# Performance work log

Hardware: AMD Instinct MI355X
Metric: run time of the kernel (lower is better)

The kernel has to match this reference:

```python
import jax, jax.numpy as jnp
import numpy as np

N_NODES = 100000
N_EDGES = 3200000
D_IN = 256
D_HID = 256
D_OUT = 64


def setup_inputs() -> dict:
    key = jax.random.key(0)
    k1, k2, k3, k4 = jax.random.split(key, 4)
    x = jax.random.normal(k1, (N_NODES, D_IN), dtype=jnp.float32)
    edge_index = jax.random.randint(k2, (2, N_EDGES), 0, N_NODES, dtype=jnp.int32)
    W1 = jax.random.normal(k3, (D_IN, D_HID), dtype=jnp.float32) / np.sqrt(D_IN)
    b1 = jnp.zeros((D_HID,), dtype=jnp.float32)
    W2 = jax.random.normal(k4, (D_HID, D_OUT), dtype=jnp.float32) / np.sqrt(D_HID)
    b2 = jnp.zeros((D_OUT,), dtype=jnp.float32)
    return {"x": x, "edge_index": edge_index, "W1": W1, "b1": b1, "W2": W2, "b2": b2}


def _gcn_conv(x, src, dst, norm, W, b, n_nodes):
    # dense linear transform, then normalized scatter-add aggregation
    h = x @ W  # [N, out]
    msg = norm[:, None] * h[src]  # gather + scale, [E+N, out]
    out = jax.ops.segment_sum(msg, dst, num_segments=n_nodes)
    return out + b


def reference(x, edge_index, W1, b1, W2, b2):
    n = x.shape[0]
    # add self-loops (PyG GCNConv default)
    loops = jnp.arange(n, dtype=edge_index.dtype)
    src = jnp.concatenate([edge_index[0], loops])
    dst = jnp.concatenate([edge_index[1], loops])
    # symmetric normalization deg^{-1/2}[src] * deg^{-1/2}[dst]
    deg = jax.ops.segment_sum(jnp.ones_like(src, dtype=x.dtype), dst, num_segments=n)
    dinv = jnp.where(deg > 0, jax.lax.rsqrt(jnp.maximum(deg, 1.0)), 0.0)
    norm = dinv[src] * dinv[dst]

    h = _gcn_conv(x, src, dst, norm, W1, b1, n)
    h = jax.nn.relu(h)
    # dropout is identity at inference
    h = _gcn_conv(h, src, dst, norm, W2, b2, n)
    return jax.nn.log_softmax(h, axis=1)
```

## Files before the change

kernel.cpp:

```cpp
#include <hip/hip_runtime.h>
#include <hip/hip_bf16.h>


typedef __bf16 bf16;
typedef bf16 bf16x4 __attribute__((ext_vector_type(4)));
typedef bf16 bf16x8 __attribute__((ext_vector_type(8)));
typedef float f32x4 __attribute__((ext_vector_type(4)));
typedef signed char s8;
typedef s8 s8x8 __attribute__((ext_vector_type(8)));

#define NBLK 256

__global__ __launch_bounds__(256) void k_b1(const int* __restrict__ edge, int E, int chunk,
                                            int NB, int* __restrict__ gcnt) {
    __shared__ int cnt[512];
    int tid = threadIdx.x;
    for (int i = tid; i < NB; i += 256) cnt[i] = 0;
    __syncthreads();
    int s = blockIdx.x * chunk, e = min(s + chunk, E);
    for (int i = s + tid; i < e; i += 256) atomicAdd(&cnt[edge[E + i] >> 9], 1);
    __syncthreads();
    for (int i = tid; i < NB; i += 256) gcnt[blockIdx.x * NB + i] = cnt[i];
}

__global__ void k_b2(const int* __restrict__ gcnt, int NB, int E, int* __restrict__ bstart) {
    __shared__ int col[256];
    int k = threadIdx.x;
    int sum = 0;
    if (k < NB)
        for (int b = 0; b < NBLK; ++b) sum += gcnt[b * NB + k];
    col[k] = sum;
    __syncthreads();
    for (int o = 1; o < 256; o <<= 1) {
        int v = (k >= o) ? col[k - o] : 0;
        __syncthreads();
        col[k] += v;
        __syncthreads();
    }
    if (k < NB) bstart[k] = col[k] - sum;
    if (k == 0) bstart[NB] = E;
}

__global__ void k_b2b(int* __restrict__ gcnt, int NB, const int* __restrict__ bstart) {
    __shared__ int col[256];
    int b = threadIdx.x;
    int k = blockIdx.x;
    int v = gcnt[b * NB + k];
    col[b] = v;
    __syncthreads();
    for (int o = 1; o < 256; o <<= 1) {
        int t = (b >= o) ? col[b - o] : 0;
        __syncthreads();
        col[b] += t;
        __syncthreads();
    }
    gcnt[b * NB + k] = bstart[k] + col[b] - v;
}

__global__ __launch_bounds__(256) void k_b3(const int* __restrict__ edge, int E, int chunk,
                                            int NB, const int* __restrict__ base,
                                            int* __restrict__ ebuf) {
    __shared__ int cnt[512];
    __shared__ int bs[512];
    int tid = threadIdx.x;
    for (int i = tid; i < NB; i += 256) {
        cnt[i] = 0;
        bs[i] = base[blockIdx.x * NB + i];
    }
    __syncthreads();
    int s = blockIdx.x * chunk, e = min(s + chunk, E);
    for (int i = s + tid; i < e; i += 256) {
        int sv = edge[i], dv = edge[E + i];
        int k = dv >> 9;
        int r = atomicAdd(&cnt[k], 1);
        ebuf[bs[k] + r] = sv | ((dv & 511) << 17);
    }
}

__global__ __launch_bounds__(256) void k_b45(const int* __restrict__ ebuf,
                                             const int* __restrict__ bstart, int n, int E,
                                             int NB, int* __restrict__ off,
                                             float* __restrict__ dinv) {
    __shared__ int cnt[512];
    __shared__ int red[256];
    int tid = threadIdx.x;
    int k = blockIdx.x;
    cnt[tid] = 0;
    cnt[tid + 256] = 0;
    __syncthreads();
    int s = bstart[k], e = bstart[k + 1];
    for (int i = s + tid; i < e; i += 256) atomicAdd(&cnt[(ebuf[i] >> 17) & 511], 1);
    __syncthreads();
    int c0 = cnt[tid * 2], c1 = cnt[tid * 2 + 1];
    int sum = c0 + c1;
    red[tid] = sum;
    __syncthreads();
    for (int o = 1; o < 256; o <<= 1) {
        int v = (tid >= o) ? red[tid - o] : 0;
        __syncthreads();
        red[tid] += v;
        __syncthreads();
    }
    int ex = red[tid] - sum;
    int base = k << 9;
    int g0 = base + tid * 2, g1 = g0 + 1;
    int o0 = s + ex, o1 = s + ex + c0;
    if (g0 < n) { off[g0] = o0; dinv[g0] = rsqrtf((float)(c0 + 1)); }
    else if (g0 == n) off[g0] = o0;
    if (g1 < n) { off[g1] = o1; dinv[g1] = rsqrtf((float)(c1 + 1)); }
    else if (g1 == n) off[g1] = o1;
    if (k == NB - 1 && tid == 0) off[n] = E;
}

__global__ __launch_bounds__(256) void k_b6(const int* __restrict__ ebuf,
                                            const int* __restrict__ bstart,
                                            const int* __restrict__ off,
                                            const float* __restrict__ dinv, int n,
                                            int2* __restrict__ pair) {
    __shared__ int cnt[512];
    __shared__ int offl[512];
    int tid = threadIdx.x;
    int k = blockIdx.x;
    int base = k << 9;
    cnt[tid] = 0;
    cnt[tid + 256] = 0;
    offl[tid] = (base + tid < n) ? off[base + tid] : 0;
    offl[tid + 256] = (base + 256 + tid < n) ? off[base + 256 + tid] : 0;
    __syncthreads();
    int s = bstart[k], e = bstart[k + 1];
    for (int i = s + tid; i < e; i += 256) {
        int pk = ebuf[i];
        int sv = pk & 0x1ffff;
        int node = (pk >> 17) & 511;
        int r = atomicAdd(&cnt[node], 1);
        pair[offl[node] + r] = make_int2(sv, __float_as_int(dinv[sv]));
    }
}

__global__ __launch_bounds__(256) void k_quant(const float* __restrict__ x,
                                               s8* __restrict__ xq,
                                               float* __restrict__ scale, int n) {
    int row = blockIdx.x * 4 + (threadIdx.x >> 6);
    int lane = threadIdx.x & 63;
    if (row >= n) return;
    f32x4 v = ((const f32x4*)x)[(size_t)row * 64 + lane];
    float m = fmaxf(fmaxf(fabsf(v[0]), fabsf(v[1])), fmaxf(fabsf(v[2]), fabsf(v[3])));
    for (int o = 32; o > 0; o >>= 1) m = fmaxf(m, __shfl_xor(m, o));
    m = fmaxf(m, 1e-20f);
    float inv = 127.0f / m;
    int b0 = __float2int_rn(v[0] * inv) & 255;
    int b1 = __float2int_rn(v[1] * inv) & 255;
    int b2 = __float2int_rn(v[2] * inv) & 255;
    int b3 = __float2int_rn(v[3] * inv) & 255;
    ((int*)xq)[(size_t)row * 64 + lane] = b0 | (b1 << 8) | (b2 << 16) | (b3 << 24);
    if (lane == 0) scale[row] = m / 127.0f;
}

__global__ __launch_bounds__(256) void k_quant2(const bf16* __restrict__ tb,
                                                s8* __restrict__ tq,
                                                float* __restrict__ tscale, int n) {
    int t = blockIdx.x * 256 + threadIdx.x;
    int row = t >> 3;
    int l8 = t & 7;
    if (row >= n) return;
    bf16x8 v = ((const bf16x8*)tb)[(size_t)row * 8 + l8];
    float f[8], m = 0.0f;
#pragma unroll
    for (int j = 0; j < 8; ++j) { f[j] = (float)v[j]; m = fmaxf(m, fabsf(f[j])); }
    for (int o = 4; o > 0; o >>= 1) m = fmaxf(m, __shfl_xor(m, o));
    m = fmaxf(m, 1e-20f);
    float inv = 127.0f / m;
    int lo = 0, hi = 0;
#pragma unroll
    for (int j = 0; j < 4; ++j) lo |= (__float2int_rn(f[j] * inv) & 255) << (8 * j);
#pragma unroll
    for (int j = 0; j < 4; ++j) hi |= (__float2int_rn(f[4 + j] * inv) & 255) << (8 * j);
    ((int2*)tq)[(size_t)row * 8 + l8] = make_int2(lo, hi);
    if (l8 == 0) tscale[row] = m / 127.0f;
}

__global__ void k_wt(const float* __restrict__ W, bf16* __restrict__ Wt, int NC) {
    int nc = blockIdx.x;
    int k = threadIdx.x;
    Wt[nc * 256 + k] = (bf16)W[k * NC + nc];
}

__global__ __launch_bounds__(256) void k_agg1(const s8* __restrict__ xq,
                                              const float* __restrict__ scale,
                                              const int* __restrict__ off,
                                              const int2* __restrict__ pair,
                                              const float* __restrict__ dinv,
                                              bf16* __restrict__ ax, int n) {
    int wv = blockIdx.x * 4 + (threadIdx.x >> 6);
    int lane = threadIdx.x & 63;
    int node = wv * 2 + (lane >> 5);
    int l32 = lane & 31;
    if (node >= n) return;
    int s0 = off[node], s1 = off[node + 1];
    float dv = dinv[node];
    const s8x8* X = (const s8x8*)xq;
    s8x8 xs = X[(size_t)node * 32 + l32];
    float ws = dv * scale[node];
    float a[8];
#pragma unroll
    for (int j = 0; j < 8; ++j) a[j] = ws * (float)xs[j];
    int e = s0;
    for (; e + 8 <= s1; e += 8) {
        int2 p[8];
#pragma unroll
        for (int q = 0; q < 8; ++q) p[q] = pair[e + q];
        float sc[8];
#pragma unroll
        for (int q = 0; q < 8; ++q) sc[q] = scale[p[q].x];
        s8x8 t[8];
#pragma unroll
        for (int q = 0; q < 8; ++q) t[q] = X[(size_t)p[q].x * 32 + l32];
#pragma unroll
        for (int q = 0; q < 8; ++q) {
            float w = __int_as_float(p[q].y) * sc[q];
#pragma unroll
            for (int j = 0; j < 8; ++j) a[j] += w * (float)t[q][j];
        }
    }
    for (; e < s1; ++e) {
        int2 p = pair[e];
        float w = __int_as_float(p.y) * scale[p.x];
        s8x8 t = X[(size_t)p.x * 32 + l32];
#pragma unroll
        for (int j = 0; j < 8; ++j) a[j] += w * (float)t[j];
    }
    bf16x8 o;
#pragma unroll
    for (int j = 0; j < 8; ++j) o[j] = (bf16)(a[j] * dv);
    ((bf16x8*)ax)[(size_t)node * 32 + l32] = o;
}

__global__ __launch_bounds__(256) void k_gemmp(const bf16* __restrict__ A,
                                               const bf16* __restrict__ Bt,
                                               const float* __restrict__ bias,
                                               bf16* __restrict__ C, int n) {
    __shared__ __align__(16) bf16 As[4 * 64 * 8];
    __shared__ __align__(16) bf16 Bs[16 * 64 * 8];
    int tid = threadIdx.x;
    int bm = blockIdx.x * 64;
    int w = tid >> 6, lane = tid & 63;

    int r = tid >> 2;
    int cq = tid & 3;
    int a_idx = (((r >> 4) * 64) + cq * 16 + (r & 15)) * 8;
    int arow = bm + r; if (arow > n - 1) arow = n - 1;

    f32x4 acc[16] = {};

    for (int k0 = 0; k0 < 256; k0 += 32) {
        __syncthreads();
        uint4 av = *(const uint4*)(A + (size_t)arow * 256 + k0 + cq * 8);
        *(uint4*)(As + a_idx) = av;
#pragma unroll
        for (int rep = 0; rep < 4; ++rep) {
            int r2 = rep * 64 + r;
            uint4 bv = *(const uint4*)(Bt + (size_t)r2 * 256 + k0 + cq * 8);
            *(uint4*)(Bs + (((r2 >> 4) * 64) + cq * 16 + (r2 & 15)) * 8) = bv;
        }
        __syncthreads();
        bf16x8 af = *(const bf16x8*)(As + (w * 64 + lane) * 8);
#pragma unroll
        for (int ct = 0; ct < 16; ++ct) {
            bf16x8 bfr = *(const bf16x8*)(Bs + (ct * 64 + lane) * 8);
            acc[ct] = __builtin_amdgcn_mfma_f32_16x16x32_bf16(af, bfr, acc[ct], 0, 0, 0);
        }
    }

    int colb = lane & 15, rowq = lane >> 4;
#pragma unroll
    for (int ct = 0; ct < 16; ++ct) {
        int col = ct * 16 + colb;
        float bv = bias[col];
#pragma unroll
        for (int rr = 0; rr < 4; ++rr) {
            int row = bm + w * 16 + rowq * 4 + rr;
            if (row < n) {
                float v = acc[ct][rr] + bv;
                C[(size_t)row * 256 + col] = (bf16)(v > 0.0f ? v : 0.0f);
            }
        }
    }
}

__global__ __launch_bounds__(256) void k_gemm2(const bf16* __restrict__ A,
                                               const bf16* __restrict__ Bt,
                                               bf16* __restrict__ C, int n) {
    __shared__ __align__(16) bf16 As[4 * 64 * 8];
    __shared__ __align__(16) bf16 Bs[4 * 64 * 8];
    int tid = threadIdx.x;
    int bm = blockIdx.x * 64;
    int w = tid >> 6, lane = tid & 63;
    int wm = w >> 1, wn = w & 1;

    int r = tid >> 2;
    int cq = tid & 3;
    int lds_idx = (((r >> 4) * 64) + cq * 16 + (r & 15)) * 8;
    int arow = bm + r; if (arow > n - 1) arow = n - 1;

    f32x4 acc[2][2] = {};

    for (int k0 = 0; k0 < 256; k0 += 32) {
        __syncthreads();
        uint4 av = *(const uint4*)(A + (size_t)arow * 256 + k0 + cq * 8);
        uint4 bv = *(const uint4*)(Bt + (size_t)r * 256 + k0 + cq * 8);
        *(uint4*)(As + lds_idx) = av;
        *(uint4*)(Bs + lds_idx) = bv;
        __syncthreads();
#pragma unroll
        for (int i = 0; i < 2; ++i) {
            bf16x8 af = *(const bf16x8*)(As + ((wm * 2 + i) * 64 + lane) * 8);
#pragma unroll
            for (int j = 0; j < 2; ++j) {
                bf16x8 bfr = *(const bf16x8*)(Bs + ((wn * 2 + j) * 64 + lane) * 8);
                acc[i][j] = __builtin_amdgcn_mfma_f32_16x16x32_bf16(af, bfr, acc[i][j], 0, 0, 0);
            }
        }
    }

    int colb = lane & 15, rowq = lane >> 4;
#pragma unroll
    for (int i = 0; i < 2; ++i) {
#pragma unroll
        for (int j = 0; j < 2; ++j) {
            int col = wn * 32 + j * 16 + colb;
#pragma unroll
            for (int rr = 0; rr < 4; ++rr) {
                int row = bm + wm * 32 + i * 16 + rowq * 4 + rr;
                if (row < n) C[(size_t)row * 64 + col] = (bf16)acc[i][j][rr];
            }
        }
    }
}

__global__ __launch_bounds__(256) void k_agg2(const s8* __restrict__ tq,
                                              const float* __restrict__ tscale,
                                              const int* __restrict__ off,
                                              const int2* __restrict__ pair,
                                              const float* __restrict__ dinv,
                                              const float* __restrict__ b2,
                                              float* __restrict__ out, int n) {
    int wv = blockIdx.x * 4 + (threadIdx.x >> 6);
    int lane = threadIdx.x & 63;
    int node = wv * 8 + (lane >> 3);
    int l8 = lane & 7;
    if (node >= n) return;
    int s0 = off[node], s1 = off[node + 1];
    float dv = dinv[node];
    const s8x8* T = (const s8x8*)tq;
    s8x8 ts = T[(size_t)node * 8 + l8];
    float ws = dv * tscale[node];
    float a[8];
#pragma unroll
    for (int j = 0; j < 8; ++j) a[j] = ws * (float)ts[j];
    int e = s0;
    for (; e + 4 <= s1; e += 4) {
        int2 p[4];
#pragma unroll
        for (int q = 0; q < 4; ++q) p[q] = pair[e + q];
        float sc[4];
#pragma unroll
        for (int q = 0; q < 4; ++q) sc[q] = tscale[p[q].x];
        s8x8 tv[4];
#pragma unroll
        for (int q = 0; q < 4; ++q) tv[q] = T[(size_t)p[q].x * 8 + l8];
#pragma unroll
        for (int q = 0; q < 4; ++q) {
            float w = __int_as_float(p[q].y) * sc[q];
#pragma unroll
            for (int j = 0; j < 8; ++j) a[j] += w * (float)tv[q][j];
        }
    }
    for (; e < s1; ++e) {
        int2 p = pair[e];
        float w = __int_as_float(p.y) * tscale[p.x];
        s8x8 tv = T[(size_t)p.x * 8 + l8];
#pragma unroll
        for (int j = 0; j < 8; ++j) a[j] += w * (float)tv[j];
    }
    const float4* B2 = (const float4*)b2;
    float4 bv0 = B2[l8 * 2], bv1 = B2[l8 * 2 + 1];
    a[0] = a[0] * dv + bv0.x; a[1] = a[1] * dv + bv0.y;
    a[2] = a[2] * dv + bv0.z; a[3] = a[3] * dv + bv0.w;
    a[4] = a[4] * dv + bv1.x; a[5] = a[5] * dv + bv1.y;
    a[6] = a[6] * dv + bv1.z; a[7] = a[7] * dv + bv1.w;
    float m = a[0];
#pragma unroll
    for (int j = 1; j < 8; ++j) m = fmaxf(m, a[j]);
    for (int o = 4; o > 0; o >>= 1) m = fmaxf(m, __shfl_xor(m, o));
    float s = 0.0f;
#pragma unroll
    for (int j = 0; j < 8; ++j) s += __expf(a[j] - m);
    for (int o = 4; o > 0; o >>= 1) s += __shfl_xor(s, o);
    float ls = m + __logf(s);
    f32x4 o0, o1;
    o0[0] = a[0] - ls; o0[1] = a[1] - ls; o0[2] = a[2] - ls; o0[3] = a[3] - ls;
    o1[0] = a[4] - ls; o1[1] = a[5] - ls; o1[2] = a[6] - ls; o1[3] = a[7] - ls;
    f32x4* O = (f32x4*)out;
    O[(size_t)node * 16 + l8 * 2] = o0;
    O[(size_t)node * 16 + l8 * 2 + 1] = o1;
}

extern "C" void kernel_launch(void* const* d_in, const int* in_sizes, int n_in,
                              void* d_out, int out_size, void* d_ws, size_t ws_size,
                              hipStream_t stream) {
    const float* x   = (const float*)d_in[0];
    const int*  edge = (const int*)d_in[1];
    const float* W1  = (const float*)d_in[2];
    const float* b1  = (const float*)d_in[3];
    const float* W2  = (const float*)d_in[4];
    const float* b2  = (const float*)d_in[5];
    float* out = (float*)d_out;

    int n = in_sizes[0] / 256;
    int E = in_sizes[1] / 2;
    int NB = (n + 511) >> 9;
    int chunk = (E + NBLK - 1) / NBLK;

    char* ws = (char*)d_ws;
    auto alloc = [&](size_t bytes) -> char* {
        char* p = ws;
        ws += (bytes + 255) & ~(size_t)255;
        return p;
    };
    int*   gcnt   = (int*)alloc((size_t)NBLK * NB * 4);
    int*   bstart = (int*)alloc((size_t)(NB + 1) * 4);
    int*   ebuf   = (int*)alloc((size_t)E * 4);
    float* dinv   = (float*)alloc((size_t)n * 4);
    int*   off    = (int*)alloc((size_t)(n + 1) * 4);
    int2*  pair   = (int2*)alloc((size_t)E * 8);
    s8*    xq     = (s8*)alloc((size_t)n * 256);
    float* scale  = (float*)alloc((size_t)n * 4);
    bf16*  ax     = (bf16*)alloc((size_t)n * 256 * 2);
    bf16*  h1     = (bf16*)alloc((size_t)n * 256 * 2);
    bf16*  tb     = (bf16*)alloc((size_t)n * 64 * 2);
    s8*    tq     = (s8*)alloc((size_t)n * 64);
    float* tscale = (float*)alloc((size_t)n * 4);
    bf16*  W1t    = (bf16*)alloc(256 * 256 * 2);
    bf16*  W2t    = (bf16*)alloc(64 * 256 * 2);

    k_b1<<<NBLK, 256, 0, stream>>>(edge, E, chunk, NB, gcnt);
    k_b2<<<1, 256, 0, stream>>>(gcnt, NB, E, bstart);
    k_b2b<<<NB, 256, 0, stream>>>(gcnt, NB, bstart);
    k_b3<<<NBLK, 256, 0, stream>>>(edge, E, chunk, NB, gcnt, ebuf);
    k_b45<<<NB, 256, 0, stream>>>(ebuf, bstart, n, E, NB, off, dinv);
    k_b6<<<NB, 256, 0, stream>>>(ebuf, bstart, off, dinv, n, pair);

    k_quant<<<(n + 3) / 4, 256, 0, stream>>>(x, xq, scale, n);
    k_wt<<<256, 256, 0, stream>>>(W1, W1t, 256);
    k_wt<<<64, 256, 0, stream>>>(W2, W2t, 64);

    k_agg1<<<(n + 7) / 8, 256, 0, stream>>>(xq, scale, off, pair, dinv, ax, n);
    k_gemmp<<<(n + 63) / 64, 256, 0, stream>>>(ax, W1t, b1, h1, n);

    k_gemm2<<<(n + 63) / 64, 256, 0, stream>>>(h1, W2t, tb, n);
    k_quant2<<<(n * 8 + 255) / 256, 256, 0, stream>>>(tb, tq, tscale, n);
    k_agg2<<<(n + 31) / 32, 256, 0, stream>>>(tq, tscale, off, pair, dinv, b2, out, n);
}
```

Before: 554.5 us.

## Fold source quant scale into edge weights and widen agg1 to 16-byte gathers

The per-source quantization scale is folded into the per-edge weight stored in the CSR pair array, which removes a random scale gather per edge in the first aggregation. The second aggregation compensates by using a per-node ratio (its scale divided by the layer-1 scale). Layer-1 features are stored as offset-by-128 unsigned bytes, the offset is subtracted once through a running weight sum, and each lane now gathers 16 bytes with four nodes per wave instead of two. The quantize kernel is moved before graph construction so the scales exist when the pair array is built. This adds a division per node and some extra float rounding from the folded weights.

```diff
diff --git a/kernel.cpp b/kernel.cpp
--- a/kernel.cpp
+++ b/kernel.cpp
@@ -115,7 +115,8 @@
 __global__ __launch_bounds__(256) void k_b6(const int* __restrict__ ebuf,
                                             const int* __restrict__ bstart,
                                             const int* __restrict__ off,
-                                            const float* __restrict__ dinv, int n,
+                                            const float* __restrict__ dinv,
+                                            const float* __restrict__ scale, int n,
                                             int2* __restrict__ pair) {
     __shared__ int cnt[512];
     __shared__ int offl[512];
@@ -133,12 +134,13 @@
         int sv = pk & 0x1ffff;
         int node = (pk >> 17) & 511;
         int r = atomicAdd(&cnt[node], 1);
-        pair[offl[node] + r] = make_int2(sv, __float_as_int(dinv[sv]));
+        float w = dinv[sv] * scale[sv];
+        pair[offl[node] + r] = make_int2(sv, __float_as_int(w));
     }
 }
 
 __global__ __launch_bounds__(256) void k_quant(const float* __restrict__ x,
-                                               s8* __restrict__ xq,
+                                               unsigned char* __restrict__ xq,
                                                float* __restrict__ scale, int n) {
     int row = blockIdx.x * 4 + (threadIdx.x >> 6);
     int lane = threadIdx.x & 63;
@@ -148,17 +150,19 @@
     for (int o = 32; o > 0; o >>= 1) m = fmaxf(m, __shfl_xor(m, o));
     m = fmaxf(m, 1e-20f);
     float inv = 127.0f / m;
-    int b0 = __float2int_rn(v[0] * inv) & 255;
-    int b1 = __float2int_rn(v[1] * inv) & 255;
-    int b2 = __float2int_rn(v[2] * inv) & 255;
-    int b3 = __float2int_rn(v[3] * inv) & 255;
+    int b0 = (__float2int_rn(v[0] * inv) + 128) & 255;
+    int b1 = (__float2int_rn(v[1] * inv) + 128) & 255;
+    int b2 = (__float2int_rn(v[2] * inv) + 128) & 255;
+    int b3 = (__float2int_rn(v[3] * inv) + 128) & 255;
     ((int*)xq)[(size_t)row * 64 + lane] = b0 | (b1 << 8) | (b2 << 16) | (b3 << 24);
     if (lane == 0) scale[row] = m / 127.0f;
 }
 
 __global__ __launch_bounds__(256) void k_quant2(const bf16* __restrict__ tb,
+                                                const float* __restrict__ scale,
                                                 s8* __restrict__ tq,
-                                                float* __restrict__ tscale, int n) {
+                                                float* __restrict__ tscale,
+                                                float* __restrict__ r2, int n) {
     int t = blockIdx.x * 256 + threadIdx.x;
     int row = t >> 3;
     int l8 = t & 7;
@@ -176,7 +180,11 @@
 #pragma unroll
     for (int j = 0; j < 4; ++j) hi |= (__float2int_rn(f[4 + j] * inv) & 255) << (8 * j);
     ((int2*)tq)[(size_t)row * 8 + l8] = make_int2(lo, hi);
-    if (l8 == 0) tscale[row] = m / 127.0f;
+    if (l8 == 0) {
+        float s = m / 127.0f;
+        tscale[row] = s;
+        r2[row] = s / scale[row];
+    }
 }
 
 __global__ void k_wt(const float* __restrict__ W, bf16* __restrict__ Wt, int NC) {
@@ -185,7 +193,28 @@
     Wt[nc * 256 + k] = (bf16)W[k * NC + nc];
 }
 
-__global__ __launch_bounds__(256) void k_agg1(const s8* __restrict__ xq,
+__device__ __forceinline__ void acc16(float a[16], uint4 t, float w, float& wsum) {
+    wsum += w;
+    unsigned u0 = t.x, u1 = t.y, u2 = t.z, u3 = t.w;
+    a[0]  += w * (float)(u0 & 255u);
+    a[1]  += w * (float)((u0 >> 8) & 255u);
+    a[2]  += w * (float)((u0 >> 16) & 255u);
+    a[3]  += w * (float)(u0 >> 24);
+    a[4]  += w * (float)(u1 & 255u);
+    a[5]  += w * (float)((u1 >> 8) & 255u);
+    a[6]  += w * (float)((u1 >> 16) & 255u);
+    a[7]  += w * (float)(u1 >> 24);
+    a[8]  += w * (float)(u2 & 255u);
+    a[9]  += w * (float)((u2 >> 8) & 255u);
+    a[10] += w * (float)((u2 >> 16) & 255u);
+    a[11] += w * (float)(u2 >> 24);
+    a[12] += w * (float)(u3 & 255u);
+    a[13] += w * (float)((u3 >> 8) & 255u);
+    a[14] += w * (float)((u3 >> 16) & 255u);
+    a[15] += w * (float)(u3 >> 24);
+}
+
+__global__ __launch_bounds__(256) void k_agg1(const unsigned char* __restrict__ xq,
                                               const float* __restrict__ scale,
                                               const int* __restrict__ off,
                                               const int2* __restrict__ pair,
@@ -193,46 +222,40 @@
                                               bf16* __restrict__ ax, int n) {
     int wv = blockIdx.x * 4 + (threadIdx.x >> 6);
     int lane = threadIdx.x & 63;
-    int node = wv * 2 + (lane >> 5);
-    int l32 = lane & 31;
+    int node = wv * 4 + (lane >> 4);
+    int l16 = lane & 15;
     if (node >= n) return;
     int s0 = off[node], s1 = off[node + 1];
     float dv = dinv[node];
-    const s8x8* X = (const s8x8*)xq;
-    s8x8 xs = X[(size_t)node * 32 + l32];
-    float ws = dv * scale[node];
-    float a[8];
-#pragma unroll
-    for (int j = 0; j < 8; ++j) a[j] = ws * (float)xs[j];
+    float a[16] = {};
+    float wsum = 0.0f;
+    uint4 xs = *(const uint4*)(xq + (size_t)node * 256 + l16 * 16);
+    acc16(a, xs, dv * scale[node], wsum);
     int e = s0;
-    for (; e + 8 <= s1; e += 8) {
-        int2 p[8];
-#pragma unroll
-        for (int q = 0; q < 8; ++q) p[q] = pair[e + q];
-        float sc[8];
-#pragma unroll
-        for (int q = 0; q < 8; ++q) sc[q] = scale[p[q].x];
-        s8x8 t[8];
-#pragma unroll
-        for (int q = 0; q < 8; ++q) t[q] = X[(size_t)p[q].x * 32 + l32];
-#pragma unroll
-        for (int q = 0; q < 8; ++q) {
-            float w = __int_as_float(p[q].y) * sc[q];
-#pragma unroll
-            for (int j = 0; j < 8; ++j) a[j] += w * (float)t[q][j];
-        }
+    for (; e + 4 <= s1; e += 4) {
+        int2 p[4];
+#pragma unroll
+        for (int q = 0; q < 4; ++q) p[q] = pair[e + q];
+        uint4 t[4];
+#pragma unroll
+        for (int q = 0; q < 4; ++q)
+            t[q] = *(const uint4*)(xq + (size_t)p[q].x * 256 + l16 * 16);
+#pragma unroll
+        for (int q = 0; q < 4; ++q) acc16(a, t[q], __int_as_float(p[q].y), wsum);
     }
     for (; e < s1; ++e) {
         int2 p = pair[e];
-        float w = __int_as_float(p.y) * scale[p.x];
-        s8x8 t = X[(size_t)p.x * 32 + l32];
-#pragma unroll
-        for (int j = 0; j < 8; ++j) a[j] += w * (float)t[j];
-    }
-    bf16x8 o;
-#pragma unroll
-    for (int j = 0; j < 8; ++j) o[j] = (bf16)(a[j] * dv);
-    ((bf16x8*)ax)[(size_t)node * 32 + l32] = o;
+        uint4 t = *(const uint4*)(xq + (size_t)p.x * 256 + l16 * 16);
+        acc16(a, t, __int_as_float(p.y), wsum);
+    }
+    float c = 128.0f * wsum;
+    bf16x8 o0, o1;
+#pragma unroll
+    for (int j = 0; j < 8; ++j) o0[j] = (bf16)((a[j] - c) * dv);
+#pragma unroll
+    for (int j = 0; j < 8; ++j) o1[j] = (bf16)((a[8 + j] - c) * dv);
+    ((bf16x8*)ax)[(size_t)node * 32 + l16 * 2] = o0;
+    ((bf16x8*)ax)[(size_t)node * 32 + l16 * 2 + 1] = o1;
 }
 
 __global__ __launch_bounds__(256) void k_gemmp(const bf16* __restrict__ A,
@@ -339,6 +362,7 @@
 
 __global__ __launch_bounds__(256) void k_agg2(const s8* __restrict__ tq,
                                               const float* __restrict__ tscale,
+                                              const float* __restrict__ r2,
                                               const int* __restrict__ off,
                                               const int2* __restrict__ pair,
                                               const float* __restrict__ dinv,
@@ -364,7 +388,7 @@
         for (int q = 0; q < 4; ++q) p[q] = pair[e + q];
         float sc[4];
 #pragma unroll
-        for (int q = 0; q < 4; ++q) sc[q] = tscale[p[q].x];
+        for (int q = 0; q < 4; ++q) sc[q] = r2[p[q].x];
         s8x8 tv[4];
 #pragma unroll
         for (int q = 0; q < 4; ++q) tv[q] = T[(size_t)p[q].x * 8 + l8];
@@ -377,7 +401,7 @@
     }
     for (; e < s1; ++e) {
         int2 p = pair[e];
-        float w = __int_as_float(p.y) * tscale[p.x];
+        float w = __int_as_float(p.y) * r2[p.x];
         s8x8 tv = T[(size_t)p.x * 8 + l8];
 #pragma unroll
         for (int j = 0; j < 8; ++j) a[j] += w * (float)tv[j];
@@ -433,31 +457,33 @@
     float* dinv   = (float*)alloc((size_t)n * 4);
     int*   off    = (int*)alloc((size_t)(n + 1) * 4);
     int2*  pair   = (int2*)alloc((size_t)E * 8);
-    s8*    xq     = (s8*)alloc((size_t)n * 256);
+    unsigned char* xq = (unsigned char*)alloc((size_t)n * 256);
     float* scale  = (float*)alloc((size_t)n * 4);
     bf16*  ax     = (bf16*)alloc((size_t)n * 256 * 2);
     bf16*  h1     = (bf16*)alloc((size_t)n * 256 * 2);
     bf16*  tb     = (bf16*)alloc((size_t)n * 64 * 2);
     s8*    tq     = (s8*)alloc((size_t)n * 64);
     float* tscale = (float*)alloc((size_t)n * 4);
+    float* r2     = (float*)alloc((size_t)n * 4);
     bf16*  W1t    = (bf16*)alloc(256 * 256 * 2);
     bf16*  W2t    = (bf16*)alloc(64 * 256 * 2);
+
+    k_quant<<<(n + 3) / 4, 256, 0, stream>>>(x, xq, scale, n);
 
     k_b1<<<NBLK, 256, 0, stream>>>(edge, E, chunk, NB, gcnt);
     k_b2<<<1, 256, 0, stream>>>(gcnt, NB, E, bstart);
     k_b2b<<<NB, 256, 0, stream>>>(gcnt, NB, bstart);
     k_b3<<<NBLK, 256, 0, stream>>>(edge, E, chunk, NB, gcnt, ebuf);
     k_b45<<<NB, 256, 0, stream>>>(ebuf, bstart, n, E, NB, off, dinv);
-    k_b6<<<NB, 256, 0, stream>>>(ebuf, bstart, off, dinv, n, pair);
-
-    k_quant<<<(n + 3) / 4, 256, 0, stream>>>(x, xq, scale, n);
+    k_b6<<<NB, 256, 0, stream>>>(ebuf, bstart, off, dinv, scale, n, pair);
+
     k_wt<<<256, 256, 0, stream>>>(W1, W1t, 256);
     k_wt<<<64, 256, 0, stream>>>(W2, W2t, 64);
 
-    k_agg1<<<(n + 7) / 8, 256, 0, stream>>>(xq, scale, off, pair, dinv, ax, n);
+    k_agg1<<<(n + 15) / 16, 256, 0, stream>>>(xq, scale, off, pair, dinv, ax, n);
     k_gemmp<<<(n + 63) / 64, 256, 0, stream>>>(ax, W1t, b1, h1, n);
 
     k_gemm2<<<(n + 63) / 64, 256, 0, stream>>>(h1, W2t, tb, n);
-    k_quant2<<<(n * 8 + 255) / 256, 256, 0, stream>>>(tb, tq, tscale, n);
-    k_agg2<<<(n + 31) / 32, 256, 0, stream>>>(tq, tscale, off, pair, dinv, b2, out, n);
-}
+    k_quant2<<<(n * 8 + 255) / 256, 256, 0, stream>>>(tb, scale, tq, tscale, r2, n);
+    k_agg2<<<(n + 31) / 32, 256, 0, stream>>>(tq, tscale, r2, off, pair, dinv, b2, out, n);
+}
```

Result: no change. 562.5 us (+1.5%).
